# Performance work log

Measured on AMD Instinct MI355X. Metric: run time of the kernel, lower is better.

## Reference

```python
import jax, jax.numpy as jnp
import numpy as np

N, DIM, T_ITERS = 8192, 64, 4

def setup_inputs() -> dict:
    key = jax.random.key(0)
    ks = jax.random.split(key, 9)
    graph = jax.random.normal(ks[0], (N, N), jnp.float32)
    x = jax.random.randint(ks[1], (N,), 0, 2, jnp.int32)  # 0/1 indicator of S
    theta1 = jax.random.normal(ks[2], (1, DIM), jnp.float32)
    theta2 = jax.random.normal(ks[3], (DIM, DIM), jnp.float32)
    theta3 = jax.random.normal(ks[4], (DIM, DIM), jnp.float32)
    theta4 = jax.random.normal(ks[5], (1, DIM), jnp.float32)
    theta5 = jax.random.normal(ks[6], (2 * DIM, 1), jnp.float32)
    theta6 = jax.random.normal(ks[7], (DIM, DIM), jnp.float32)
    theta7 = jax.random.normal(ks[8], (DIM, DIM), jnp.float32)
    return dict(graph=graph, x=x, theta1=theta1, theta2=theta2, theta3=theta3,
                theta4=theta4, theta5=theta5, theta6=theta6, theta7=theta7,
                v=100, T=T_ITERS)


def reference(graph, x, theta1, theta2, theta3, theta4, theta5, theta6, theta7, v, T):
    dt = graph.dtype
    xf = x.astype(dt)  # (N,)
    # c_v = sum_u relu(theta4 * graph[v,u]) @ theta3.
    # Exact identity: relu(t*w) = max(w,0)*relu(t) + max(-w,0)*relu(-t),
    s_pos = jnp.maximum(graph, 0.0).sum(axis=1)   # (N,)
    s_neg = jnp.maximum(-graph, 0.0).sum(axis=1)  # (N,)
    t4 = theta4[0]  # (dim,)
    c = (s_pos[:, None] * jax.nn.relu(t4)
         + s_neg[:, None] * jax.nn.relu(-t4)) @ theta3  # (N, dim)
    a = xf[:, None] * theta1  # (N, dim) via broadcast of (1, dim)

    def step(u, _):
        summ = u.sum(axis=0, keepdims=True)        # (1, dim)
        b = (summ - u) @ theta2                    # (N, dim)
        return jax.nn.relu(a + b + c), None

    u0 = jnp.zeros((graph.shape[0], theta1.shape[1]), dt)
    u, _ = jax.lax.scan(step, u0, None, length=T)

    summ = u.sum(axis=0)                           # (dim,)
    q_in = jnp.concatenate([summ @ theta6, u[v] @ theta7])  # (2*dim,)
    return jax.nn.relu(q_in) @ theta5              # (1,)
```

## Files before the change

### kernel.cpp

```cpp
#include <hip/hip_runtime.h>

#define NN 8192
#define DIM 64
#define T_IT 4
#define NPART 8

typedef float nfloat4 __attribute__((ext_vector_type(4)));

__global__ void prep_kernel(const float* __restrict__ theta3,
                            const float* __restrict__ theta4,
                            float* __restrict__ pq,
                            float* __restrict__ summ1_parts,
                            float* __restrict__ summ) {
  const int d = threadIdx.x;
  float p = 0.f, q = 0.f;
  for (int k = 0; k < DIM; ++k) {
    const float t4 = theta4[k];
    const float th = theta3[k * DIM + d];
    p += fmaxf(t4, 0.f) * th;
    q += fmaxf(-t4, 0.f) * th;
  }
  pq[d] = p;
  pq[DIM + d] = q;
#pragma unroll
  for (int c = 0; c < NPART; ++c) summ1_parts[c * DIM + d] = 0.f;
#pragma unroll
  for (int t = 0; t < T_IT - 1; ++t) summ[t * DIM + d] = 0.f;
}

__global__ __launch_bounds__(256) void fused_rowsum_step1(
    const float* __restrict__ graph, const int* __restrict__ x,
    const float* __restrict__ theta1, const float* __restrict__ pq,
    float* __restrict__ s_pos, float* __restrict__ s_neg,
    float* __restrict__ u, float* __restrict__ summ1_parts) {
  const int wave = threadIdx.x >> 6;
  const int lane = threadIdx.x & 63;
  const int row = blockIdx.x * 4 + wave;
  const float pd = pq[lane];
  const float qd = pq[DIM + lane];
  const float t1d = theta1[lane];

  const nfloat4* g = (const nfloat4*)(graph + (size_t)row * NN);
  float sp = 0.f, sn = 0.f;
  for (int it = 0; it < NN / 4 / 64; it += 8) {
#pragma unroll
    for (int j = 0; j < 8; ++j) {
      const nfloat4 v = __builtin_nontemporal_load(&g[lane + (it + j) * 64]);
      sp += fmaxf(v.x, 0.f) + fmaxf(v.y, 0.f) + fmaxf(v.z, 0.f) + fmaxf(v.w, 0.f);
      sn += fmaxf(-v.x, 0.f) + fmaxf(-v.y, 0.f) + fmaxf(-v.z, 0.f) + fmaxf(-v.w, 0.f);
    }
  }
#pragma unroll
  for (int off = 32; off > 0; off >>= 1) {
    sp += __shfl_down(sp, off);
    sn += __shfl_down(sn, off);
  }
  sp = __shfl(sp, 0);
  sn = __shfl(sn, 0);
  if (lane == 0) {
    s_pos[row] = sp;
    s_neg[row] = sn;
  }
  const float uv = fmaxf((float)x[row] * t1d + sp * pd + sn * qd, 0.f);
  u[(size_t)row * DIM + lane] = uv;

  __shared__ float red[4][DIM];
  red[wave][lane] = uv;
  __syncthreads();
  if (wave == 0)
    atomicAdd(&summ1_parts[(blockIdx.x & (NPART - 1)) * DIM + lane],
              red[0][lane] + red[1][lane] + red[2][lane] + red[3][lane]);
}

__global__ __launch_bounds__(256) void step_kernel(
    const float* __restrict__ theta1, const float* __restrict__ theta2,
    const int* __restrict__ x, const float* __restrict__ s_pos,
    const float* __restrict__ s_neg, const float* __restrict__ pq,
    const float* __restrict__ summ_in, int ncopies,
    float* __restrict__ summ_out, float* __restrict__ u) {
  __shared__ float th2[DIM * DIM];
  __shared__ float sin_sh[DIM];
  __shared__ float gsh[DIM];
  __shared__ __align__(16) float ush[4][DIM];
  __shared__ float red[4][DIM];
  const int t = threadIdx.x;
  const int d = t & 63;
  const int r = t >> 6;

  for (int i = t; i < DIM * DIM; i += 256) th2[i] = theta2[i];
  if (t < DIM) {
    float s = 0.f;
    for (int c = 0; c < ncopies; ++c) s += summ_in[c * DIM + t];
    sin_sh[t] = s;
  }
  __syncthreads();
  if (t < DIM) {
    float g = 0.f;
    for (int k = 0; k < DIM; ++k) g += sin_sh[k] * th2[k * DIM + d];
    gsh[d] = g;
  }
  const float pd = pq[d];
  const float qd = pq[DIM + d];
  const float t1d = theta1[d];
  __syncthreads();
  const float gd = gsh[d];

  float acc = 0.f;
  for (int base = blockIdx.x * 4; base < NN; base += gridDim.x * 4) {
    const int row = base + r;
    ush[r][d] = u[(size_t)row * DIM + d];
    __syncthreads();
    float dot = 0.f;
    const float4* ur = (const float4*)ush[r];
#pragma unroll
    for (int kk = 0; kk < DIM / 4; ++kk) {
      const float4 uv = ur[kk];
      dot += uv.x * th2[(4 * kk + 0) * DIM + d];
      dot += uv.y * th2[(4 * kk + 1) * DIM + d];
      dot += uv.z * th2[(4 * kk + 2) * DIM + d];
      dot += uv.w * th2[(4 * kk + 3) * DIM + d];
    }
    const float acv = (float)x[row] * t1d + s_pos[row] * pd + s_neg[row] * qd;
    float val = fmaxf(acv + gd - dot, 0.f);
    u[(size_t)row * DIM + d] = val;
    acc += val;
    __syncthreads();
  }
  red[r][d] = acc;
  __syncthreads();
  if (r == 0) {
    atomicAdd(&summ_out[d], red[0][d] + red[1][d] + red[2][d] + red[3][d]);
  }
}

__global__ void final_kernel(const float* __restrict__ theta5,
                             const float* __restrict__ theta6,
                             const float* __restrict__ theta7,
                             const float* __restrict__ summ,
                             const float* __restrict__ u,
                             const int* __restrict__ vptr,
                             float* __restrict__ out) {
  const int t = threadIdx.x;
  const int d = t & 63;
  float h;
  if (t < DIM) {
    float s = 0.f;
    for (int k = 0; k < DIM; ++k) s += summ[k] * theta6[k * DIM + d];
    h = fmaxf(s, 0.f) * theta5[d];
  } else {
    const int v = *vptr;
    const float* uv = u + (size_t)v * DIM;
    float s = 0.f;
    for (int k = 0; k < DIM; ++k) s += uv[k] * theta7[k * DIM + d];
    h = fmaxf(s, 0.f) * theta5[DIM + d];
  }
  __shared__ float red[128];
  red[t] = h;
  __syncthreads();
  if (t == 0) {
    float s = 0.f;
    for (int i = 0; i < 128; ++i) s += red[i];
    out[0] = s;
  }
}

extern "C" void kernel_launch(void* const* d_in, const int* in_sizes, int n_in,
                              void* d_out, int out_size, void* d_ws, size_t ws_size,
                              hipStream_t stream) {
  const float* graph  = (const float*)d_in[0];
  const int*   x      = (const int*)d_in[1];
  const float* theta1 = (const float*)d_in[2];
  const float* theta2 = (const float*)d_in[3];
  const float* theta3 = (const float*)d_in[4];
  const float* theta4 = (const float*)d_in[5];
  const float* theta5 = (const float*)d_in[6];
  const float* theta6 = (const float*)d_in[7];
  const float* theta7 = (const float*)d_in[8];
  const int*   vptr   = (const int*)d_in[9];
  float* out = (float*)d_out;

  float* ws     = (float*)d_ws;
  float* pq     = ws;
  float* parts  = ws + 128;
  float* summ   = ws + 128 + NPART * DIM;
  float* s_pos  = summ + (T_IT - 1) * DIM;
  float* s_neg  = s_pos + NN;
  float* u      = s_neg + NN;

  prep_kernel<<<1, DIM, 0, stream>>>(theta3, theta4, pq, parts, summ);
  fused_rowsum_step1<<<2048, 256, 0, stream>>>(graph, x, theta1, pq,
                                               s_pos, s_neg, u, parts);
  step_kernel<<<256, 256, 0, stream>>>(theta1, theta2, x, s_pos, s_neg, pq,
                                       parts, NPART, summ + 0 * DIM, u);
  for (int t = 2; t < T_IT; ++t) {
    step_kernel<<<256, 256, 0, stream>>>(theta1, theta2, x, s_pos, s_neg, pq,
                                         summ + (t - 2) * DIM, 1,
                                         summ + (t - 1) * DIM, u);
  }
  final_kernel<<<1, 128, 0, stream>>>(theta5, theta6, theta7,
                                      summ + (T_IT - 2) * DIM, u, vptr, out);
}
```

Baseline: 408.9 us.

## Keep theta2 columns in registers and drop per-row block barriers in step kernel

```diff
diff --git a/kernel.cpp b/kernel.cpp
--- a/kernel.cpp
+++ b/kernel.cpp
@@ -78,58 +78,56 @@
     const float* __restrict__ s_neg, const float* __restrict__ pq,
     const float* __restrict__ summ_in, int ncopies,
     float* __restrict__ summ_out, float* __restrict__ u) {
-  __shared__ float th2[DIM * DIM];
   __shared__ float sin_sh[DIM];
-  __shared__ float gsh[DIM];
-  __shared__ __align__(16) float ush[4][DIM];
+  __shared__ __align__(16) float ulds[4][DIM];
   __shared__ float red[4][DIM];
   const int t = threadIdx.x;
-  const int d = t & 63;
-  const int r = t >> 6;
-
-  for (int i = t; i < DIM * DIM; i += 256) th2[i] = theta2[i];
+  const int lane = t & 63;
+  const int wave = t >> 6;
+
+  float th2col[DIM];
+#pragma unroll
+  for (int k = 0; k < DIM; ++k) th2col[k] = theta2[k * DIM + lane];
+
   if (t < DIM) {
     float s = 0.f;
     for (int c = 0; c < ncopies; ++c) s += summ_in[c * DIM + t];
     sin_sh[t] = s;
   }
-  __syncthreads();
-  if (t < DIM) {
-    float g = 0.f;
-    for (int k = 0; k < DIM; ++k) g += sin_sh[k] * th2[k * DIM + d];
-    gsh[d] = g;
-  }
-  const float pd = pq[d];
-  const float qd = pq[DIM + d];
-  const float t1d = theta1[d];
-  __syncthreads();
-  const float gd = gsh[d];
-
+  const float pd = pq[lane];
+  const float qd = pq[DIM + lane];
+  const float t1d = theta1[lane];
+  __syncthreads();
+  float gd = 0.f;
+#pragma unroll
+  for (int k = 0; k < DIM; ++k) gd += sin_sh[k] * th2col[k];
+
+  const int gwave = blockIdx.x * 4 + wave;
+  const int nwaves = gridDim.x * 4;
   float acc = 0.f;
-  for (int base = blockIdx.x * 4; base < NN; base += gridDim.x * 4) {
-    const int row = base + r;
-    ush[r][d] = u[(size_t)row * DIM + d];
-    __syncthreads();
+  for (int row = gwave; row < NN; row += nwaves) {
+    const float uval = u[(size_t)row * DIM + lane];
+    ulds[wave][lane] = uval;
     float dot = 0.f;
-    const float4* ur = (const float4*)ush[r];
+    const float4* ur = (const float4*)ulds[wave];
 #pragma unroll
     for (int kk = 0; kk < DIM / 4; ++kk) {
       const float4 uv = ur[kk];
-      dot += uv.x * th2[(4 * kk + 0) * DIM + d];
-      dot += uv.y * th2[(4 * kk + 1) * DIM + d];
-      dot += uv.z * th2[(4 * kk + 2) * DIM + d];
-      dot += uv.w * th2[(4 * kk + 3) * DIM + d];
+      dot += uv.x * th2col[4 * kk + 0];
+      dot += uv.y * th2col[4 * kk + 1];
+      dot += uv.z * th2col[4 * kk + 2];
+      dot += uv.w * th2col[4 * kk + 3];
     }
     const float acv = (float)x[row] * t1d + s_pos[row] * pd + s_neg[row] * qd;
-    float val = fmaxf(acv + gd - dot, 0.f);
-    u[(size_t)row * DIM + d] = val;
+    const float val = fmaxf(acv + gd - dot, 0.f);
+    u[(size_t)row * DIM + lane] = val;
     acc += val;
-    __syncthreads();
-  }
-  red[r][d] = acc;
-  __syncthreads();
-  if (r == 0) {
-    atomicAdd(&summ_out[d], red[0][d] + red[1][d] + red[2][d] + red[3][d]);
+  }
+  red[wave][lane] = acc;
+  __syncthreads();
+  if (wave == 0) {
+    atomicAdd(&summ_out[lane],
+              red[0][lane] + red[1][lane] + red[2][lane] + red[3][lane]);
   }
 }
 
@@ -190,12 +188,12 @@
   prep_kernel<<<1, DIM, 0, stream>>>(theta3, theta4, pq, parts, summ);
   fused_rowsum_step1<<<2048, 256, 0, stream>>>(graph, x, theta1, pq,
                                                s_pos, s_neg, u, parts);
-  step_kernel<<<256, 256, 0, stream>>>(theta1, theta2, x, s_pos, s_neg, pq,
-                                       parts, NPART, summ + 0 * DIM, u);
+  step_kernel<<<1024, 256, 0, stream>>>(theta1, theta2, x, s_pos, s_neg, pq,
+                                        parts, NPART, summ + 0 * DIM, u);
   for (int t = 2; t < T_IT; ++t) {
-    step_kernel<<<256, 256, 0, stream>>>(theta1, theta2, x, s_pos, s_neg, pq,
-                                         summ + (t - 2) * DIM, 1,
-                                         summ + (t - 1) * DIM, u);
+    step_kernel<<<1024, 256, 0, stream>>>(theta1, theta2, x, s_pos, s_neg, pq,
+                                          summ + (t - 2) * DIM, 1,
+                                          summ + (t - 1) * DIM, u);
   }
   final_kernel<<<1, 128, 0, stream>>>(theta5, theta6, theta7,
                                       summ + (T_IT - 2) * DIM, u, vptr, out);
```

New measurement: 448.2 us. 1.1x slower.
